# Kernel tuning notes

Hardware: AMD Instinct MI355X
Metric: run time of the kernel (lower is better)

Reference implementation:

```python
import jax, jax.numpy as jnp
import numpy as np

B, N, DEG = 256, 16384, 32  # batch, num_neurons, fan-in per neuron

def setup_inputs() -> dict:
    key = jax.random.key(0)
    kx, kw, ki = jax.random.split(key, 3)
    x = jax.random.normal(kx, (B, N), dtype=jnp.float32)
    w = jax.random.normal(kw, (N, DEG), dtype=jnp.float32)  # nonzero weights per neuron
    idx = jax.random.randint(ki, (N, DEG), 0, N)            # source-neuron indices per neuron
    return {"x": x, "w": w, "idx": idx}

def reference(x, w, idx):
    # Per neuron j: gather its fan-in channels and apply Dense(1) with
    # kernel = nonzero weights, then relu; concat over neurons == axis N.
    gathered = x[:, idx]                      # [B, N, DEG] gather
    out = jnp.einsum('bnd,nd->bn', gathered, w)  # sparse matvec per batch row
    return jax.nn.relu(out)                   # [B, N]
```

## Files before the change

### kernel.cpp

```cpp
#include <hip/hip_runtime.h>


#define NB   16384
#define DEG  32

typedef __fp16 hp2 __attribute__((ext_vector_type(2)));

__device__ __forceinline__ unsigned pk16(float a, float b) {
    return __builtin_bit_cast(unsigned, (hp2)__builtin_amdgcn_cvt_pkrtz(a, b));
}

__global__ __launch_bounds__(256) void prep_pw_kernel(
    const int* __restrict__ idx, const float* __restrict__ w,
    uint4* __restrict__ pw4) {
    __shared__ int   idx_s[64][33];
    __shared__ float w_s[64][33];
    const int t  = threadIdx.x;
    const int nb = (int)blockIdx.x * 64;

    const int4*   src  = (const int4*)(idx + (size_t)nb * DEG);
    const float4* srcw = (const float4*)(w   + (size_t)nb * DEG);
#pragma unroll
    for (int p = 0; p < 2; ++p) {
        const int e4 = t + 256 * p;
        const int n0 = e4 >> 3;
        const int c0 = (e4 & 7) * 4;
        const int4 v = src[e4];
        idx_s[n0][c0 + 0] = v.x; idx_s[n0][c0 + 1] = v.y;
        idx_s[n0][c0 + 2] = v.z; idx_s[n0][c0 + 3] = v.w;
        const float4 f = srcw[e4];
        w_s[n0][c0 + 0] = f.x; w_s[n0][c0 + 1] = f.y;
        w_s[n0][c0 + 2] = f.z; w_s[n0][c0 + 3] = f.w;
    }
    __syncthreads();

    const int np    = t & 63;
    const int dbase = t >> 6;
#pragma unroll
    for (int k = 0; k < 2; ++k) {
        const int d4 = dbase * 2 + k;
        const int c  = 4 * d4;
        uint4 o;
        o.x = (unsigned)idx_s[np][c + 0] | ((unsigned)idx_s[np][c + 1] << 16);
        o.y = pk16(w_s[np][c + 0], w_s[np][c + 1]);
        o.z = (unsigned)idx_s[np][c + 2] | ((unsigned)idx_s[np][c + 3] << 16);
        o.w = pk16(w_s[np][c + 2], w_s[np][c + 3]);
        pw4[(size_t)d4 * NB + nb + np] = o;
    }
}

#define LOADQ(buf, nn)                                                     \
    do {                                                                   \
        const uint4* p_ = pw4 + (nn);                                      \
        _Pragma("unroll") for (int d4_ = 0; d4_ < 8; ++d4_)                \
            buf[d4_] = p_[(size_t)d4_ * NB];                               \
    } while (0)

#define ACC2(buf, D4, r01, r23)                                            \
    {                                                                      \
        const unsigned jpA = buf[D4].x;                                    \
        const uint2 gA0 = lds[jpA & 0xffffu];                              \
        const uint2 gA1 = lds[jpA >> 16];                                  \
        const hp2 wA  = __builtin_bit_cast(hp2, buf[D4].y);                \
        const hp2 wAlo = {wA.x, wA.x};                                     \
        const hp2 wAhi = {wA.y, wA.y};                                     \
        r01 += wAlo * __builtin_bit_cast(hp2, gA0.x);                      \
        r23 += wAlo * __builtin_bit_cast(hp2, gA0.y);                      \
        r01 += wAhi * __builtin_bit_cast(hp2, gA1.x);                      \
        r23 += wAhi * __builtin_bit_cast(hp2, gA1.y);                      \
        const unsigned jpB = buf[D4].z;                                    \
        const uint2 gB0 = lds[jpB & 0xffffu];                              \
        const uint2 gB1 = lds[jpB >> 16];                                  \
        const hp2 wB  = __builtin_bit_cast(hp2, buf[D4].w);                \
        const hp2 wBlo = {wB.x, wB.x};                                     \
        const hp2 wBhi = {wB.y, wB.y};                                     \
        r01 += wBlo * __builtin_bit_cast(hp2, gB0.x);                      \
        r23 += wBlo * __builtin_bit_cast(hp2, gB0.y);                      \
        r01 += wBhi * __builtin_bit_cast(hp2, gB1.x);                      \
        r23 += wBhi * __builtin_bit_cast(hp2, gB1.y);                      \
    }

#define STEP(CUR, NXT, I, PF)                                              \
    {                                                                      \
        const int n = n0 + t + 1024 * (I);                                 \
        if (PF) LOADQ(NXT, n + 1024);                                      \
        hp2 a01 = {0, 0}, a23 = {0, 0}, c01 = {0, 0}, c23 = {0, 0};        \
        ACC2(CUR, 0, a01, a23)                                             \
        ACC2(CUR, 1, a01, a23)                                             \
        ACC2(CUR, 2, a01, a23)                                             \
        ACC2(CUR, 3, a01, a23)                                             \
        ACC2(CUR, 4, c01, c23)                                             \
        ACC2(CUR, 5, c01, c23)                                             \
        ACC2(CUR, 6, c01, c23)                                             \
        ACC2(CUR, 7, c01, c23)                                             \
        const hp2 s01 = a01 + c01;                                         \
        const hp2 s23 = a23 + c23;                                         \
        __builtin_nontemporal_store(fmaxf((float)s01.x, 0.f),              \
                                    &out[(size_t)(b0 + 0) * NB + n]);      \
        __builtin_nontemporal_store(fmaxf((float)s01.y, 0.f),              \
                                    &out[(size_t)(b0 + 1) * NB + n]);      \
        __builtin_nontemporal_store(fmaxf((float)s23.x, 0.f),              \
                                    &out[(size_t)(b0 + 2) * NB + n]);      \
        __builtin_nontemporal_store(fmaxf((float)s23.y, 0.f),              \
                                    &out[(size_t)(b0 + 3) * NB + n]);      \
    }

__global__ __launch_bounds__(1024, 4) void gather4_kernel(
    const float* __restrict__ x, const uint4* __restrict__ pw4,
    float* __restrict__ out) {
    extern __shared__ uint2 lds[];
    const int t  = threadIdx.x;
    const int q  = (int)blockIdx.x & 63;
    const int n0 = ((int)blockIdx.x >> 6) * 4096;

    const float* xr0 = x + (size_t)(4 * q) * NB;
    const float* xr1 = xr0 + NB;
    const float* xr2 = xr1 + NB;
    const float* xr3 = xr2 + NB;
#pragma unroll
    for (int p = 0; p < 4; ++p) {
        const int j = 4 * (t + 1024 * p);
        const float4 r0 = *(const float4*)&xr0[j];
        const float4 r1 = *(const float4*)&xr1[j];
        const float4 r2 = *(const float4*)&xr2[j];
        const float4 r3 = *(const float4*)&xr3[j];
        uint4 w0, w1;
        w0.x = pk16(r0.x, r1.x); w0.y = pk16(r2.x, r3.x);
        w0.z = pk16(r0.y, r1.y); w0.w = pk16(r2.y, r3.y);
        w1.x = pk16(r0.z, r1.z); w1.y = pk16(r2.z, r3.z);
        w1.z = pk16(r0.w, r1.w); w1.w = pk16(r2.w, r3.w);
        *(uint4*)&lds[j]     = w0;
        *(uint4*)&lds[j + 2] = w1;
    }

    uint4 U[8], V[8];
    LOADQ(U, n0 + t);
    __syncthreads();

    const int b0 = 4 * q;
    STEP(U, V, 0, 1)
    STEP(V, U, 1, 1)
    STEP(U, V, 2, 1)
    STEP(V, U, 3, 0)
}

extern "C" void kernel_launch(void* const* d_in, const int* in_sizes, int n_in,
                              void* d_out, int out_size, void* d_ws, size_t ws_size,
                              hipStream_t stream) {
    const float* x   = (const float*)d_in[0];
    const float* w   = (const float*)d_in[1];
    const int*   idx = (const int*)d_in[2];
    float* out = (float*)d_out;
    uint4* pw4 = (uint4*)d_ws;

    (void)hipFuncSetAttribute((const void*)gather4_kernel,
                              hipFuncAttributeMaxDynamicSharedMemorySize, 131072);

    prep_pw_kernel<<<NB / 64, 256, 0, stream>>>(idx, w, pw4);

    gather4_kernel<<<256, 1024, 131072, stream>>>(x, pw4, out);
}
```

Before: 83.36 us.

## Fuse weight/index packing and gather into one cooperative kernel with grid sync

Merges the prep kernel that packs indices and fp16 weights with the gather kernel into a single cooperative launch. Each block packs 64 neurons, stages its x image into LDS, then waits on a grid-wide barrier before running the gather. This removes one kernel launch and lets the x staging overlap with the packing, at the cost of a grid sync and a fallback path if the cooperative launch fails. It requires all 256 blocks of 1024 threads with 128KB LDS to be co-resident.

```diff
diff --git a/kernel.cpp b/kernel.cpp
--- a/kernel.cpp
+++ b/kernel.cpp
@@ -1,4 +1,7 @@
 #include <hip/hip_runtime.h>
+#include <hip/hip_cooperative_groups.h>
+
+namespace cg = cooperative_groups;
 
 
 #define NB   16384
@@ -10,44 +13,6 @@
     return __builtin_bit_cast(unsigned, (hp2)__builtin_amdgcn_cvt_pkrtz(a, b));
 }
 
-__global__ __launch_bounds__(256) void prep_pw_kernel(
-    const int* __restrict__ idx, const float* __restrict__ w,
-    uint4* __restrict__ pw4) {
-    __shared__ int   idx_s[64][33];
-    __shared__ float w_s[64][33];
-    const int t  = threadIdx.x;
-    const int nb = (int)blockIdx.x * 64;
-
-    const int4*   src  = (const int4*)(idx + (size_t)nb * DEG);
-    const float4* srcw = (const float4*)(w   + (size_t)nb * DEG);
-#pragma unroll
-    for (int p = 0; p < 2; ++p) {
-        const int e4 = t + 256 * p;
-        const int n0 = e4 >> 3;
-        const int c0 = (e4 & 7) * 4;
-        const int4 v = src[e4];
-        idx_s[n0][c0 + 0] = v.x; idx_s[n0][c0 + 1] = v.y;
-        idx_s[n0][c0 + 2] = v.z; idx_s[n0][c0 + 3] = v.w;
-        const float4 f = srcw[e4];
-        w_s[n0][c0 + 0] = f.x; w_s[n0][c0 + 1] = f.y;
-        w_s[n0][c0 + 2] = f.z; w_s[n0][c0 + 3] = f.w;
-    }
-    __syncthreads();
-
-    const int np    = t & 63;
-    const int dbase = t >> 6;
-#pragma unroll
-    for (int k = 0; k < 2; ++k) {
-        const int d4 = dbase * 2 + k;
-        const int c  = 4 * d4;
-        uint4 o;
-        o.x = (unsigned)idx_s[np][c + 0] | ((unsigned)idx_s[np][c + 1] << 16);
-        o.y = pk16(w_s[np][c + 0], w_s[np][c + 1]);
-        o.z = (unsigned)idx_s[np][c + 2] | ((unsigned)idx_s[np][c + 3] << 16);
-        o.w = pk16(w_s[np][c + 2], w_s[np][c + 3]);
-        pw4[(size_t)d4 * NB + nb + np] = o;
-    }
-}
 
 #define LOADQ(buf, nn)                                                     \
     do {                                                                   \
@@ -105,6 +70,123 @@
                                     &out[(size_t)(b0 + 3) * NB + n]);      \
     }
 
+#define STAGE_X_IMAGE()                                                    \
+    {                                                                      \
+        const float* xr0 = x + (size_t)(4 * q) * NB;                       \
+        const float* xr1 = xr0 + NB;                                       \
+        const float* xr2 = xr1 + NB;                                       \
+        const float* xr3 = xr2 + NB;                                       \
+        _Pragma("unroll") for (int p = 0; p < 4; ++p) {                    \
+            const int j = 4 * (t + 1024 * p);                              \
+            const float4 r0 = *(const float4*)&xr0[j];                     \
+            const float4 r1 = *(const float4*)&xr1[j];                     \
+            const float4 r2 = *(const float4*)&xr2[j];                     \
+            const float4 r3 = *(const float4*)&xr3[j];                     \
+            uint4 w0, w1;                                                  \
+            w0.x = pk16(r0.x, r1.x); w0.y = pk16(r2.x, r3.x);              \
+            w0.z = pk16(r0.y, r1.y); w0.w = pk16(r2.y, r3.y);              \
+            w1.x = pk16(r0.z, r1.z); w1.y = pk16(r2.z, r3.z);              \
+            w1.z = pk16(r0.w, r1.w); w1.w = pk16(r2.w, r3.w);              \
+            *(uint4*)&lds[j]     = w0;                                     \
+            *(uint4*)&lds[j + 2] = w1;                                     \
+        }                                                                  \
+    }
+
+
+__global__ __launch_bounds__(1024, 4) void fused_kernel(
+    const float* __restrict__ x, const int* __restrict__ idx,
+    const float* __restrict__ w, uint4* __restrict__ pw4,
+    float* __restrict__ out) {
+    extern __shared__ uint2 lds[];
+    const int t   = threadIdx.x;
+    const int bid = (int)blockIdx.x;
+    const int q   = bid & 63;
+    const int n0  = (bid >> 6) * 4096;
+
+    {
+        int*   idx_s = (int*)lds;
+        float* w_s   = (float*)lds + 64 * 33;
+        const int nb = bid * 64;
+        if (t < 512) {
+            const int4   v = ((const int4*)(idx + (size_t)nb * DEG))[t];
+            const float4 f = ((const float4*)(w  + (size_t)nb * DEG))[t];
+            const int nr = t >> 3;
+            const int c0 = (t & 7) * 4;
+            idx_s[nr * 33 + c0 + 0] = v.x; idx_s[nr * 33 + c0 + 1] = v.y;
+            idx_s[nr * 33 + c0 + 2] = v.z; idx_s[nr * 33 + c0 + 3] = v.w;
+            w_s[nr * 33 + c0 + 0] = f.x; w_s[nr * 33 + c0 + 1] = f.y;
+            w_s[nr * 33 + c0 + 2] = f.z; w_s[nr * 33 + c0 + 3] = f.w;
+        }
+        __syncthreads();
+        if (t < 512) {
+            const int np = t & 63;
+            const int d4 = t >> 6;
+            const int c  = 4 * d4;
+            uint4 o;
+            o.x = (unsigned)idx_s[np * 33 + c + 0] |
+                  ((unsigned)idx_s[np * 33 + c + 1] << 16);
+            o.y = pk16(w_s[np * 33 + c + 0], w_s[np * 33 + c + 1]);
+            o.z = (unsigned)idx_s[np * 33 + c + 2] |
+                  ((unsigned)idx_s[np * 33 + c + 3] << 16);
+            o.w = pk16(w_s[np * 33 + c + 2], w_s[np * 33 + c + 3]);
+            pw4[(size_t)d4 * NB + nb + np] = o;
+        }
+        __syncthreads();
+    }
+
+    STAGE_X_IMAGE();
+
+    cg::this_grid().sync();
+
+    uint4 U[8], V[8];
+    LOADQ(U, n0 + t);
+    const int b0 = 4 * q;
+    STEP(U, V, 0, 1)
+    STEP(V, U, 1, 1)
+    STEP(U, V, 2, 1)
+    STEP(V, U, 3, 0)
+}
+
+
+__global__ __launch_bounds__(256) void prep_pw_kernel(
+    const int* __restrict__ idx, const float* __restrict__ w,
+    uint4* __restrict__ pw4) {
+    __shared__ int   idx_s[64][33];
+    __shared__ float w_s[64][33];
+    const int t  = threadIdx.x;
+    const int nb = (int)blockIdx.x * 64;
+
+    const int4*   src  = (const int4*)(idx + (size_t)nb * DEG);
+    const float4* srcw = (const float4*)(w   + (size_t)nb * DEG);
+#pragma unroll
+    for (int p = 0; p < 2; ++p) {
+        const int e4 = t + 256 * p;
+        const int n0 = e4 >> 3;
+        const int c0 = (e4 & 7) * 4;
+        const int4 v = src[e4];
+        idx_s[n0][c0 + 0] = v.x; idx_s[n0][c0 + 1] = v.y;
+        idx_s[n0][c0 + 2] = v.z; idx_s[n0][c0 + 3] = v.w;
+        const float4 f = srcw[e4];
+        w_s[n0][c0 + 0] = f.x; w_s[n0][c0 + 1] = f.y;
+        w_s[n0][c0 + 2] = f.z; w_s[n0][c0 + 3] = f.w;
+    }
+    __syncthreads();
+
+    const int np    = t & 63;
+    const int dbase = t >> 6;
+#pragma unroll
+    for (int k = 0; k < 2; ++k) {
+        const int d4 = dbase * 2 + k;
+        const int c  = 4 * d4;
+        uint4 o;
+        o.x = (unsigned)idx_s[np][c + 0] | ((unsigned)idx_s[np][c + 1] << 16);
+        o.y = pk16(w_s[np][c + 0], w_s[np][c + 1]);
+        o.z = (unsigned)idx_s[np][c + 2] | ((unsigned)idx_s[np][c + 3] << 16);
+        o.w = pk16(w_s[np][c + 2], w_s[np][c + 3]);
+        pw4[(size_t)d4 * NB + nb + np] = o;
+    }
+}
+
 __global__ __launch_bounds__(1024, 4) void gather4_kernel(
     const float* __restrict__ x, const uint4* __restrict__ pw4,
     float* __restrict__ out) {
@@ -113,25 +195,7 @@
     const int q  = (int)blockIdx.x & 63;
     const int n0 = ((int)blockIdx.x >> 6) * 4096;
 
-    const float* xr0 = x + (size_t)(4 * q) * NB;
-    const float* xr1 = xr0 + NB;
-    const float* xr2 = xr1 + NB;
-    const float* xr3 = xr2 + NB;
-#pragma unroll
-    for (int p = 0; p < 4; ++p) {
-        const int j = 4 * (t + 1024 * p);
-        const float4 r0 = *(const float4*)&xr0[j];
-        const float4 r1 = *(const float4*)&xr1[j];
-        const float4 r2 = *(const float4*)&xr2[j];
-        const float4 r3 = *(const float4*)&xr3[j];
-        uint4 w0, w1;
-        w0.x = pk16(r0.x, r1.x); w0.y = pk16(r2.x, r3.x);
-        w0.z = pk16(r0.y, r1.y); w0.w = pk16(r2.y, r3.y);
-        w1.x = pk16(r0.z, r1.z); w1.y = pk16(r2.z, r3.z);
-        w1.z = pk16(r0.w, r1.w); w1.w = pk16(r2.w, r3.w);
-        *(uint4*)&lds[j]     = w0;
-        *(uint4*)&lds[j + 2] = w1;
-    }
+    STAGE_X_IMAGE();
 
     uint4 U[8], V[8];
     LOADQ(U, n0 + t);
@@ -153,10 +217,18 @@
     float* out = (float*)d_out;
     uint4* pw4 = (uint4*)d_ws;
 
+    (void)hipFuncSetAttribute((const void*)fused_kernel,
+                              hipFuncAttributeMaxDynamicSharedMemorySize, 131072);
     (void)hipFuncSetAttribute((const void*)gather4_kernel,
                               hipFuncAttributeMaxDynamicSharedMemorySize, 131072);
 
-    prep_pw_kernel<<<NB / 64, 256, 0, stream>>>(idx, w, pw4);
-
-    gather4_kernel<<<256, 1024, 131072, stream>>>(x, pw4, out);
-}
+    void* args[5] = {(void*)&x, (void*)&idx, (void*)&w, (void*)&pw4, (void*)&out};
+    hipError_t e = hipLaunchCooperativeKernel((const void*)fused_kernel,
+                                              dim3(256), dim3(1024), args,
+                                              131072, stream);
+    if (e != hipSuccess) {
+        (void)hipGetLastError();
+        prep_pw_kernel<<<NB / 64, 256, 0, stream>>>(idx, w, pw4);
+        gather4_kernel<<<256, 1024, 131072, stream>>>(x, pw4, out);
+    }
+}
```

Result: slower. 126.6 us (+51.8%).
